# Kernel tuning notes

Hardware: AMD Instinct MI355X
Metric: run time of the kernel (lower is better)

Reference implementation:

```python
import jax, jax.numpy as jnp
import numpy as np

B, C_IN, C_OUT, N, T = 32, 64, 192, 307, 24
DILATIONS = (1, 2)
O3 = C_OUT // 3  # out channels per branch


def setup_inputs() -> dict:
    key = jax.random.key(0)
    ks = iter(jax.random.split(key, 32))
    nrm = lambda shape: 0.05 * jax.random.normal(next(ks), shape, dtype=jnp.float32)
    return {
        "x": jax.random.normal(next(ks), (B, C_IN, N, T), dtype=jnp.float32),
        "adj": jax.random.randint(next(ks), (N, N), 0, 2, dtype=jnp.int32),
        "ln_g": jnp.ones((T,), jnp.float32),
        "ln_b": jnp.zeros((T,), jnp.float32),
        "res_W": nrm((C_OUT, C_IN)), "res_b": nrm((C_OUT,)),
        "ca_W1": nrm((T,)), "ca_W2": nrm((N, T)), "ca_W3": nrm((N,)),
        "cc_W": nrm((O3, C_IN)), "cc_b": nrm((O3,)),
        "ta_W1": nrm((N,)), "ta_W2": nrm((C_IN, N)), "ta_W3": nrm((C_IN,)),
        "tc_W0": nrm((O3, C_IN, 1, 2)), "tc_b0": nrm((O3,)),
        "tc_W1": nrm((O3, O3, 1, 2)), "tc_b1": nrm((O3,)),
        "ga_W1": nrm((T,)), "ga_W2": nrm((C_IN, T)), "ga_W3": nrm((C_IN,)),
        "g_W": nrm((O3, C_IN)),
    }


def layer_norm_lastdim(x, g, b, eps=1e-5):
    mu = jnp.mean(x, axis=-1, keepdims=True)
    var = jnp.var(x, axis=-1, keepdims=True)
    return (x - mu) * jax.lax.rsqrt(var + eps) * g + b


def conv1x1(x, W, b):
    # x: [B,C,N,T], W: [O,C]
    return jnp.einsum("oc,bcnt->bont", W, x) + b[None, :, None, None]


def c_attention(x, W1, W2, W3):
    # channel attention over C; x: [B,C,N,T]
    lhs = jnp.einsum("bcn,nt->bct", jnp.einsum("bcnt,t->bcn", x, W1), W2)  # [B,C,T]
    rhs = jnp.einsum("n,bcnt->bct", W3, x)                                  # [B,C,T]
    att = jax.nn.softmax(jnp.einsum("bct,bdt->bcd", lhs, rhs), axis=-1)     # [B,C,C]
    return jnp.einsum("bcd,bdnt->bcnt", att, x)


def t_attention(x, W1, W2, W3):
    # temporal attention over T; x: [B,C,N,T]
    lhs = jnp.einsum("bct,cn->btn", jnp.einsum("bcnt,n->bct", x, W1), W2)   # [B,T,N]
    rhs = jnp.einsum("c,bcnt->bnt", W3, x)                                   # [B,N,T]
    att = jax.nn.softmax(jnp.einsum("btn,bns->bts", lhs, rhs), axis=-1)      # [B,T,T]
    return jnp.einsum("bts,bcns->bcnt", att, x)


def g_attention(x, adj, W1, W2, W3):
    # graph (spatial) attention over N, masked by adjacency; x: [B,C,N,T]
    lhs = jnp.einsum("bcn,ct->bnt", jnp.einsum("bcnt,t->bcn", x, W1), W2)   # [B,N,T]
    rhs = jnp.einsum("c,bcnt->bnt", W3, x)                                   # [B,N,T]
    scores = jnp.einsum("bnt,bmt->bnm", lhs, rhs)                            # [B,N,N]
    scores = jnp.where(adj[None] > 0, scores, jnp.float32(-1e30))
    att = jax.nn.softmax(scores, axis=-1)
    return jnp.einsum("bnm,bcmt->bcnt", att, x)


def causal_conv(x, W, b, d):
    # Conv2d kernel [1,2], dilation [1,d], pad [0,d] + Chomp(d) == left-pad-only causal conv
    y = jax.lax.conv_general_dilated(
        x, W, window_strides=(1, 1), padding=((0, 0), (d, 0)),
        rhs_dilation=(1, d), dimension_numbers=("NCHW", "OIHW", "NCHW"))
    return y + b[None, :, None, None]


def meam_forward(x, adj, ln_g, ln_b, res_W, res_b, ca_W1, ca_W2, ca_W3, cc_W, cc_b,
                 ta_W1, ta_W2, ta_W3, tc_W0, tc_b0, tc_W1, tc_b1,
                 ga_W1, ga_W2, ga_W3, g_W):
    h = layer_norm_lastdim(x, ln_g, ln_b)
    # CACN branch: channel attention + 1x1 conv
    c_out = conv1x1(c_attention(h, ca_W1, ca_W2, ca_W3), cc_W, cc_b)
    # TACN branch: temporal attention + dilated causal convs
    t_out = t_attention(h, ta_W1, ta_W2, ta_W3)
    t_out = causal_conv(t_out, tc_W0, tc_b0, DILATIONS[0])
    t_out = causal_conv(t_out, tc_W1, tc_b1, DILATIONS[1])
    # GACN branch: graph attention + channel mixing
    g_out = jnp.einsum("oc,bcnt->bont", g_W, g_attention(h, adj, ga_W1, ga_W2, ga_W3))
    out = jnp.concatenate([c_out, t_out, g_out], axis=1)  # [B, C_OUT, N, T]
    return jax.nn.relu(out + conv1x1(x, res_W, res_b))


def reference(x, adj, ln_g, ln_b, res_W, res_b, ca_W1, ca_W2, ca_W3, cc_W, cc_b,
              ta_W1, ta_W2, ta_W3, tc_W0, tc_b0, tc_W1, tc_b1,
              ga_W1, ga_W2, ga_W3, g_W):
    return meam_forward(x, adj, ln_g, ln_b, res_W, res_b, ca_W1, ca_W2, ca_W3, cc_W, cc_b,
                        ta_W1, ta_W2, ta_W3, tc_W0, tc_b0, tc_W1, tc_b1,
                        ga_W1, ga_W2, ga_W3, g_W)
```

## Files before the change

### kernel.cpp

```cpp
#include <hip/hip_runtime.h>
#include <hip/hip_bf16.h>

#define BB 32
#define CC 64
#define NN 307
#define TT 24
#define CO 192
#define NT (NN*TT)
#define GO 1536

using bf16 = __hip_bfloat16;
typedef __attribute__((ext_vector_type(8))) short bf16x8;
typedef __attribute__((ext_vector_type(4))) float f32x4;

#define OFF_ln_g   0
#define OFF_ln_b   24
#define OFF_res_W  48
#define OFF_res_b  12336
#define OFF_ca_W1  12528
#define OFF_ca_W2  12552
#define OFF_ca_W3  19920
#define OFF_cc_W   20227
#define OFF_cc_b   24323
#define OFF_ta_W1  24387
#define OFF_ta_W2  24694
#define OFF_ta_W3  44342
#define OFF_tc_W0  44406
#define OFF_tc_b0  52598
#define OFF_tc_W1  52662
#define OFF_tc_b1  60854
#define OFF_ga_W1  60918
#define OFF_ga_W2  60942
#define OFF_ga_W3  62478
#define OFF_g_W    62542
#define W_TOTAL    66638

__device__ __forceinline__ float xload(const void* p, size_t i, int f) {
  return f ? ((const float*)p)[i] : __bfloat162float(((const bf16*)p)[i]);
}
__device__ __forceinline__ void ostore(void* p, size_t i, float v, int f) {
  if (f) ((float*)p)[i] = v; else ((bf16*)p)[i] = __float2bfloat16(v);
}
__device__ __forceinline__ float oload(const void* p, size_t i, int f) {
  return f ? ((const float*)p)[i] : __bfloat162float(((const bf16*)p)[i]);
}

__global__ void MEAM_44787918963464_kernel() {}

__global__ __launch_bounds__(256) void k_probe(const void* lng_raw, int* flag) {
  if (threadIdx.x == 0 && blockIdx.x == 0) {
    unsigned w = *(const unsigned*)lng_raw;
    *flag = (w == 0x3F800000u) ? 1 : 0;
  }
}

__global__ __launch_bounds__(256) void k_cvt_w(
    const void* p0, const void* p1, const void* p2, const void* p3,
    const void* p4, const void* p5, const void* p6, const void* p7,
    const void* p8, const void* p9, const void* p10, const void* p11,
    const void* p12, const void* p13, const void* p14, const void* p15,
    const void* p16, const void* p17, const void* p18, const void* p19,
    const int* flagp, float* dst) {
  int i = blockIdx.x*256 + threadIdx.x;
  if (i >= W_TOTAL) return;
  const void* ps[20] = {p0,p1,p2,p3,p4,p5,p6,p7,p8,p9,p10,p11,p12,p13,p14,p15,p16,p17,p18,p19};
  const int sz[20] = {24,24,12288,192,24,7368,307,4096,64,307,19648,64,8192,64,8192,64,24,1536,64,4096};
  int f = *flagp;
  int s = 0, base = 0;
  while (i >= base + sz[s]) { base += sz[s]; s++; }
  dst[i] = f ? ((const float*)ps[s])[i-base]
             : __bfloat162float(((const bf16*)ps[s])[i-base]);
}

__global__ __launch_bounds__(256) void k_prep_tc(const float* __restrict__ W,
    bf16* __restrict__ Ag, float* __restrict__ tb_bias) {
  int g = blockIdx.x*256 + threadIdx.x;
  if (g >= CC*CC) return;
  int pI = g >> 6, c = g & 63;
  const float* W0 = W + OFF_tc_W0;
  const float* b0 = W + OFF_tc_b0;
  const float* W1 = W + OFF_tc_W1;
  const float* b1 = W + OFF_tc_b1;
  const float* resW = W + OFF_res_W;
  const float* resb = W + OFF_res_b;
  float m0=0.f,m1=0.f,m2=0.f,m3=0.f, bb0=0.f, bb2=0.f;
  for (int o=0;o<CC;o++){
    float a1v = W1[(pI*CC+o)*2], b1v = W1[(pI*CC+o)*2+1];
    float a0v = W0[(o*CC+c)*2],  b0v = W0[(o*CC+c)*2+1];
    m0 += b1v*b0v; m1 += b1v*a0v; m2 += a1v*b0v; m3 += a1v*a0v;
    bb0 += b1v*b0[o]; bb2 += a1v*b0[o];
  }
  Ag[pI*320 + 0*64 + c] = __float2bfloat16(m0);
  Ag[pI*320 + 1*64 + c] = __float2bfloat16(m1);
  Ag[pI*320 + 2*64 + c] = __float2bfloat16(m2);
  Ag[pI*320 + 3*64 + c] = __float2bfloat16(m3);
  Ag[pI*320 + 4*64 + c] = __float2bfloat16(resW[(64+pI)*CC + c]);
  if (c == 0){
    tb_bias[pI]    = b1[pI] + bb0 + resb[64+pI];
    tb_bias[64+pI] = bb2;
  }
}

__global__ __launch_bounds__(256) void k_prep_A(const float* __restrict__ Mc,
    const float* __restrict__ W, bf16* __restrict__ Apre) {
  int idx = blockIdx.x*256 + threadIdx.x;
  if (idx >= BB*192*128) return;
  int b = idx / 24576;
  int rem = idx - b*24576;
  int p2 = rem >> 7, k = rem & 127;
  const float* resW = W + OFF_res_W;
  const float* gW   = W + OFF_g_W;
  float v;
  if (p2 < 64)       v = (k < 64) ? Mc[b*CC*CC + p2*CC + k] : resW[p2*CC + (k-64)];
  else if (p2 < 128) v = (k < 64) ? gW[(p2-64)*CC + k] : 0.f;
  else               v = (k < 64) ? 0.f : resW[p2*CC + (k-64)];
  Apre[idx] = __float2bfloat16(v);
}

__global__ __launch_bounds__(256) void k_lnct(const void* __restrict__ x, const int* flagp,
    const float* __restrict__ W,
    float* __restrict__ mu_a, float* __restrict__ rs_a,
    float* __restrict__ xw1c, float* __restrict__ xw1g,
    float* __restrict__ lhsc, float* __restrict__ rhsc, float* __restrict__ xw1t) {
  int bc = blockIdx.x;
  int tid = threadIdx.x;
  int f = *flagp;
  const float* lng  = W + OFF_ln_g;
  const float* lnb  = W + OFF_ln_b;
  const float* caW1 = W + OFF_ca_W1;
  const float* gaW1 = W + OFF_ga_W1;
  const float* caW2 = W + OFF_ca_W2;
  const float* caW3 = W + OFF_ca_W3;
  const float* taW1 = W + OFF_ta_W1;
  __shared__ float xs[NN*25];
  __shared__ float mus[NN], rss[NN], w1c[NN];
  __shared__ float red[3*240];
  size_t base = (size_t)bc * NT;
  if (f) {
    const float4* xp = (const float4*)((const float*)x + base);
    for (int e=tid; e<NT/4; e+=256){
      float4 q = xp[e];
      int n = e/6; int t0 = e*4 - n*24;
      float* d = &xs[n*25 + t0];
      d[0]=q.x; d[1]=q.y; d[2]=q.z; d[3]=q.w;
    }
  } else {
    const uint4* xp = (const uint4*)((const unsigned short*)x + base);
    for (int e=tid; e<NT/8; e+=256){
      uint4 q = xp[e]; unsigned u[4]={q.x,q.y,q.z,q.w};
      int n = e/3; int t0 = e*8 - n*24;
      float* d = &xs[n*25 + t0];
      #pragma unroll
      for (int k=0;k<4;k++){
        union{unsigned uu;float fl;} lo,hi;
        lo.uu=u[k]<<16; hi.uu=u[k]&0xffff0000u;
        d[k*2]=lo.fl; d[k*2+1]=hi.fl;
      }
    }
  }
  __syncthreads();
  for (int n=tid; n<NN; n+=256){
    const float* row = &xs[n*25];
    float mu=0.f;
    #pragma unroll
    for (int t=0;t<TT;t++) mu += row[t];
    mu *= (1.f/TT);
    float var=0.f;
    #pragma unroll
    for (int t=0;t<TT;t++){ float d=row[t]-mu; var += d*d; }
    var *= (1.f/TT);
    float rs = rsqrtf(var+1e-5f);
    float s1=0.f, s2=0.f;
    #pragma unroll
    for (int t=0;t<TT;t++){
      float hv=(row[t]-mu)*rs*lng[t]+lnb[t];
      s1+=hv*caW1[t]; s2+=hv*gaW1[t];
    }
    mus[n]=mu; rss[n]=rs; w1c[n]=s1;
    int gi = bc*NN+n;
    mu_a[gi]=mu; rs_a[gi]=rs; xw1c[gi]=s1; xw1g[gi]=s2;
  }
  __syncthreads();
  int t = tid % TT, g = tid / TT;
  if (g < 10){
    float gt=lng[t], bt=lnb[t];
    float l=0.f, rr=0.f, xt=0.f;
    for (int n=g; n<NN; n+=10){
      float hv=(xs[n*25+t]-mus[n])*rss[n]*gt+bt;
      l += w1c[n]*caW2[n*TT+t];
      rr+= caW3[n]*hv;
      xt+= taW1[n]*hv;
    }
    red[g*TT+t]=l; red[240+g*TT+t]=rr; red[480+g*TT+t]=xt;
  }
  __syncthreads();
  if (tid < TT){
    float L=0.f,R=0.f,X=0.f;
    #pragma unroll
    for (int g2=0; g2<10; g2++){
      L+=red[g2*TT+tid]; R+=red[240+g2*TT+tid]; X+=red[480+g2*TT+tid];
    }
    lhsc[bc*TT+tid]=L; rhsc[bc*TT+tid]=R; xw1t[bc*TT+tid]=X;
  }
}

__global__ __launch_bounds__(256) void k_prep_bn(const void* __restrict__ x, const int* flagp,
    const float* __restrict__ mu_a, const float* __restrict__ rs_a,
    const float* __restrict__ W, const float* __restrict__ xw1g,
    float* __restrict__ rhst, float* __restrict__ rhsg, float* __restrict__ lhsg) {
  int i = blockIdx.x*256 + threadIdx.x;
  if (i >= BB*NN*TT) return;
  int f = *flagp;
  const float* lng  = W + OFF_ln_g;
  const float* lnb  = W + OFF_ln_b;
  const float* taW3 = W + OFF_ta_W3;
  const float* gaW3 = W + OFF_ga_W3;
  const float* gaW2 = W + OFF_ga_W2;
  int t = i % TT; int n = (i/TT)%NN; int b = i/(NN*TT);
  float gt = lng[t], bt = lnb[t];
  float a=0.f,c2=0.f,d=0.f;
  for (int c=0;c<CC;c++){
    int row = (b*CC+c)*NN + n;
    float hv = (xload(x, (size_t)row*TT+t, f) - mu_a[row]) * rs_a[row] * gt + bt;
    a  += taW3[c]*hv;
    c2 += gaW3[c]*hv;
    d  += xw1g[row]*gaW2[c*TT+t];
  }
  rhst[i]=a; rhsg[i]=c2; lhsg[i]=d;
}

__global__ __launch_bounds__(256) void k_lhs_t(const float* __restrict__ xw1t,
    const float* __restrict__ W, float* __restrict__ lhst) {
  int i = blockIdx.x*256 + threadIdx.x;
  if (i >= BB*TT*NN) return;
  const float* taW2 = W + OFF_ta_W2;
  int n = i % NN; int t = (i/NN)%TT; int b = i/(TT*NN);
  float acc=0.f;
  for (int c=0;c<CC;c++)
    acc += xw1t[(b*CC+c)*TT+t]*taW2[c*NN+n];
  lhst[i]=acc;
}

__global__ __launch_bounds__(256) void k_att_c(const float* __restrict__ lhsc,
    const float* __restrict__ rhsc, const float* __restrict__ W,
    float* __restrict__ Mc) {
  int b = blockIdx.x; int tid = threadIdx.x;
  const float* ccW = W + OFF_cc_W;
  __shared__ float lc[CC*TT], rc[CC*TT], sc[CC*(CC+1)];
  for (int e=tid;e<CC*TT;e+=256){
    lc[e]=lhsc[b*CC*TT+e];
    rc[e]=rhsc[b*CC*TT+e];
  }
  __syncthreads();
  for (int e=tid;e<CC*CC;e+=256){
    int c=e>>6, d=e&63; float s=0.f;
    for (int t=0;t<TT;t++) s += lc[c*TT+t]*rc[d*TT+t];
    sc[c*(CC+1)+d]=s;
  }
  __syncthreads();
  if (tid<CC){
    float mx=-1e30f;
    for (int d=0;d<CC;d++) mx=fmaxf(mx, sc[tid*(CC+1)+d]);
    float sum=0.f;
    for (int d=0;d<CC;d++){ float e2=__expf(sc[tid*(CC+1)+d]-mx); sc[tid*(CC+1)+d]=e2; sum+=e2; }
    float inv=1.f/sum;
    for (int d=0;d<CC;d++) sc[tid*(CC+1)+d]*=inv;
  }
  __syncthreads();
  for (int e=tid;e<CC*CC;e+=256){
    int o=e>>6, d=e&63; float acc=0.f;
    for (int c=0;c<CC;c++) acc += ccW[o*CC+c]*sc[c*(CC+1)+d];
    Mc[b*CC*CC+e]=acc;
  }
}

__global__ __launch_bounds__(256) void k_att_t(const float* __restrict__ lhst,
    const float* __restrict__ rhst, float* __restrict__ attt) {
  int b=blockIdx.x, tid=threadIdx.x;
  __shared__ float sc[TT*TT];
  for (int e=tid;e<TT*TT;e+=256){
    int t=e/TT, s=e%TT;
    float acc=0.f;
    for (int n=0;n<NN;n++)
      acc += lhst[(b*TT+t)*NN+n]*rhst[(b*NN+n)*TT+s];
    sc[e]=acc;
  }
  __syncthreads();
  if (tid < TT){
    float mx=-1e30f;
    for (int s=0;s<TT;s++) mx=fmaxf(mx,sc[tid*TT+s]);
    float sum=0.f;
    for (int s=0;s<TT;s++){ float e=__expf(sc[tid*TT+s]-mx); sc[tid*TT+s]=e; sum+=e; }
    float inv=1.f/sum;
    for (int s=0;s<TT;s++) attt[b*TT*TT + tid*TT + s]=sc[tid*TT+s]*inv;
  }
}

__global__ __launch_bounds__(256) void k_scores_g(const float* __restrict__ lhsg,
    const float* __restrict__ rhsg, const int* __restrict__ adj,
    float* __restrict__ Sg) {
  int mt = blockIdx.x, nt = blockIdx.y, b = blockIdx.z;
  int n0 = nt*64, m0 = mt*64, tid = threadIdx.x;
  __shared__ unsigned short Lh[64*40], Ll[64*40], Rh[64*40], Rl[64*40];
  for (int e=tid; e<64*24; e+=256){
    int r=e/24, t=e-(e/24)*24;
    int gn=n0+r, gm=m0+r;
    float lv = (gn<NN)? lhsg[((size_t)b*NN+gn)*TT+t] : 0.f;
    float rv = (gm<NN)? rhsg[((size_t)b*NN+gm)*TT+t] : 0.f;
    bf16 lh=__float2bfloat16(lv); float lhf=__bfloat162float(lh);
    bf16 llo=__float2bfloat16(lv-lhf);
    bf16 rh=__float2bfloat16(rv); float rhf=__bfloat162float(rh);
    bf16 rlo=__float2bfloat16(rv-rhf);
    Lh[r*40+t]=*(unsigned short*)&lh; Ll[r*40+t]=*(unsigned short*)&llo;
    Rh[r*40+t]=*(unsigned short*)&rh; Rl[r*40+t]=*(unsigned short*)&rlo;
  }
  for (int e=tid; e<64*8; e+=256){
    int r=e>>3, t=24+(e&7);
    Lh[r*40+t]=0; Ll[r*40+t]=0; Rh[r*40+t]=0; Rl[r*40+t]=0;
  }
  __syncthreads();
  int lane=tid&63, w=tid>>6, q=lane>>4, lr=lane&15;
  bf16x8 ah = *(const bf16x8*)&Lh[(w*16+lr)*40 + q*8];
  bf16x8 al = *(const bf16x8*)&Ll[(w*16+lr)*40 + q*8];
  f32x4 z4={0.f,0.f,0.f,0.f};
  f32x4 acc[4]={z4,z4,z4,z4};
  #pragma unroll
  for (int ct=0;ct<4;ct++){
    bf16x8 bh = *(const bf16x8*)&Rh[(ct*16+lr)*40 + q*8];
    bf16x8 bl = *(const bf16x8*)&Rl[(ct*16+lr)*40 + q*8];
    acc[ct]=__builtin_amdgcn_mfma_f32_16x16x32_bf16(ah,bh,acc[ct],0,0,0);
    acc[ct]=__builtin_amdgcn_mfma_f32_16x16x32_bf16(ah,bl,acc[ct],0,0,0);
    acc[ct]=__builtin_amdgcn_mfma_f32_16x16x32_bf16(al,bh,acc[ct],0,0,0);
  }
  #pragma unroll
  for (int ct=0;ct<4;ct++){
    int m = m0 + ct*16 + lr;
    #pragma unroll
    for (int r=0;r<4;r++){
      int n = n0 + w*16 + q*4 + r;
      if (n<NN && m<NN){
        float s = acc[ct][r];
        if (adj[n*NN+m] <= 0) s = -1e30f;
        Sg[((size_t)b*NN+n)*NN+m] = s;
      }
    }
  }
}

__global__ __launch_bounds__(256) void k_smax_g(const float* __restrict__ Sg,
    bf16* __restrict__ attgh) {
  int b = blockIdx.y;
  int n = blockIdx.x*4 + (threadIdx.x>>6);
  int lane = threadIdx.x & 63;
  if (n >= NN) return;
  const float* row = Sg + ((size_t)b*NN+n)*NN;
  float v[5]; float mx = -1e30f;
  #pragma unroll
  for (int i=0;i<5;i++){
    int m = lane + i*64;
    v[i] = (m<NN)? row[m] : -1e30f;
    mx = fmaxf(mx, v[i]);
  }
  #pragma unroll
  for (int off=32; off; off>>=1) mx = fmaxf(mx, __shfl_xor(mx, off));
  float sum = 0.f;
  #pragma unroll
  for (int i=0;i<5;i++){
    int m = lane + i*64;
    float e = (m<NN)? __expf(v[i]-mx) : 0.f;
    v[i]=e; sum += e;
  }
  #pragma unroll
  for (int off=32; off; off>>=1) sum += __shfl_xor(sum, off);
  float inv = 1.f/sum;
  bf16* orow = attgh + ((size_t)b*NN+n)*NN;
  #pragma unroll
  for (int i=0;i<5;i++){
    int m = lane + i*64;
    if (m<NN) orow[m] = __float2bfloat16(v[i]*inv);
  }
}

__global__ __launch_bounds__(256) void k_hgc_mfma(
    const void* __restrict__ x, const int* flagp,
    const float* __restrict__ mu_a, const float* __restrict__ rs_a,
    const float* __restrict__ W, const bf16* __restrict__ Apre,
    bf16* __restrict__ hg, bf16* __restrict__ resg, void* __restrict__ out) {
  int jt = blockIdx.x, b = blockIdx.y, tid = threadIdx.x;
  int f = *flagp;
  int j0 = jt*64;
  const float* lng = W + OFF_ln_g;
  const float* lnb = W + OFF_ln_b;
  const float* ccb = W + OFF_cc_b;
  const float* resb= W + OFF_res_b;
  __shared__ unsigned short Bs[64*128];

  {
    int c = tid >> 2, jg = tid & 3;
    float xv[16];
    int jbase = j0 + jg*16;
    size_t xoff = (size_t)(b*CC + c)*NT + jbase;
    if (jbase + 15 < NT) {
      if (f) {
        const float4* xp = (const float4*)((const float*)x + xoff);
        #pragma unroll
        for (int v=0; v<4; v++){ float4 q = xp[v]; xv[v*4]=q.x; xv[v*4+1]=q.y; xv[v*4+2]=q.z; xv[v*4+3]=q.w; }
      } else {
        const uint4* xp = (const uint4*)((const unsigned short*)x + xoff);
        #pragma unroll
        for (int v=0; v<2; v++){
          uint4 q = xp[v]; unsigned u[4]={q.x,q.y,q.z,q.w};
          #pragma unroll
          for (int kk2=0;kk2<4;kk2++){
            union{unsigned uu;float fl;} lo,hi;
            lo.uu=u[kk2]<<16; hi.uu=u[kk2]&0xffff0000u;
            xv[v*8+kk2*2]=lo.fl; xv[v*8+kk2*2+1]=hi.fl;
          }
        }
      }
    } else {
      #pragma unroll
      for (int i=0;i<16;i++){ int j=jbase+i; xv[i] = (j<NT)? xload(x, xoff+i, f) : 0.f; }
    }
    const float* mu_r = mu_a + (b*CC+c)*NN;
    const float* rs_r = rs_a + (b*CC+c)*NN;
    #pragma unroll
    for (int i=0;i<16;i++){
      int j = jbase + i;
      int jl = jg*16 + i;
      float hv = 0.f, xf = 0.f;
      if (j < NT){
        int n = j / 24, t = j - n*24;
        xf = xv[i];
        hv = (xf - mu_r[n]) * rs_r[n] * lng[t] + lnb[t];
      }
      int cs = c ^ ((jl&7)<<3);
      bf16 hb = __float2bfloat16(hv), xb = __float2bfloat16(xf);
      Bs[jl*128 + cs]      = *(unsigned short*)&hb;
      Bs[jl*128 + cs + 64] = *(unsigned short*)&xb;
    }
  }

  int lane = tid & 63, w = tid >> 6;
  int q = lane >> 4, lr = lane & 15;
  bf16x8 afo[4], afh[2], afr[2];
  {
    const unsigned short* Ab = (const unsigned short*)Apre + (size_t)b*24576;
    const unsigned short* r0 = Ab + (w*16 + lr)*128;
    #pragma unroll
    for (int kc=0;kc<4;kc++) afo[kc] = *(const bf16x8*)&r0[kc*32 + q*8];
    const unsigned short* r1 = Ab + (64 + w*16 + lr)*128;
    #pragma unroll
    for (int kc=0;kc<2;kc++) afh[kc] = *(const bf16x8*)&r1[kc*32 + q*8];
    const unsigned short* r2 = Ab + (128 + w*16 + lr)*128;
    #pragma unroll
    for (int kc=0;kc<2;kc++) afr[kc] = *(const bf16x8*)&r2[(kc+2)*32 + q*8];
  }
  f32x4 z4 = {0.f,0.f,0.f,0.f};
  f32x4 acco[4] = {z4,z4,z4,z4};
  f32x4 acch[4] = {z4,z4,z4,z4};
  f32x4 accr[4] = {z4,z4,z4,z4};
  __syncthreads();

// ... 461 lines not shown
      bf16x8 bfr = *(const bf16x8*)&Xs[(nl*24+t)*64 + cb];
      acc[ct] = __builtin_amdgcn_mfma_f32_16x16x32_bf16(af[8+kc2], bfr, acc[ct], 0,0,0);
    }
  }

  #pragma unroll
  for (int ct=0;ct<12;ct++){
    int col = ct*16 + lr;
    int nl = col/24, t = col - nl*24;
    int nn = n0 + nl;
    if (nn < NN){
      #pragma unroll
      for (int r=0;r<4;r++){
        int pI = w*16 + q*4 + r;
        size_t idx = ((size_t)b*CO + 64 + pI)*NT + (size_t)nn*TT + t;
        float v = acc[ct][r] + tb_bias[pI] + (t>=2 ? tb_bias[64+pI] : 0.f);
        ostore(out, idx, fmaxf(v, 0.f), f);
      }
    }
  }
}

__global__ __launch_bounds__(256) void k_res_final(const void* __restrict__ x, const int* flagp,
    const float* __restrict__ W, void* __restrict__ out) {
  int jt=blockIdx.x, ot=blockIdx.y, b=blockIdx.z; int tid=threadIdx.x;
  int f = *flagp;
  int j0=jt*64, o0=ot*64;
  const float* resW = W + OFF_res_W;
  const float* resb = W + OFF_res_b;
  __shared__ float Ws[CC*64];
  __shared__ float Xs[CC*64];
  for (int e=tid;e<CC*64;e+=256){
    int o=e&63, c=e>>6;
    Ws[e] = resW[(o0+o)*CC + c];
  }
  for (int e=tid;e<CC*64;e+=256){
    int c=e>>6, j=e&63; int jj=j0+j;
    Xs[e] = (jj<NT) ? xload(x, (size_t)(b*CC+c)*NT + jj, f) : 0.f;
  }
  __syncthreads();
  int ti=tid&15, tj=tid>>4;
  float acc[4][4]={};
  for (int k=0;k<CC;k++){
    float4 a4=*(const float4*)&Ws[k*64+ti*4];
    float4 b4=*(const float4*)&Xs[k*64+tj*4];
    float av[4]={a4.x,a4.y,a4.z,a4.w};
    float bv[4]={b4.x,b4.y,b4.z,b4.w};
    for (int i=0;i<4;i++)
      for (int j=0;j<4;j++) acc[i][j]+=av[i]*bv[j];
  }
  for (int i=0;i<4;i++){
    int o=o0+ti*4+i; float bias=resb[o];
    for (int j=0;j<4;j++){
      int jj=j0+tj*4+j;
      if (jj<NT){
        size_t idx=((size_t)b*CO+o)*NT+jj;
        float v = acc[i][j] + bias + oload(out, idx, f);
        ostore(out, idx, fmaxf(v,0.f), f);
      }
    }
  }
}

extern "C" void kernel_launch(void* const* d_in, const int* in_sizes, int n_in,
                              void* d_out, int out_size, void* d_ws, size_t ws_size,
                              hipStream_t stream) {
  const void* x     = d_in[0];
  const int*  adj   = (const int*)d_in[1];
  void* out = d_out;

  float* p = (float*)d_ws;
  int*   flagp = (int*)p; p += 4;
  float* Wf  = p; p += W_TOTAL;
  float* mu_a = p; p += (size_t)BB*CC*NN;
  float* rs_a = p; p += (size_t)BB*CC*NN;
  float* xw1c = p; p += (size_t)BB*CC*NN;
  float* xw1g = p; p += (size_t)BB*CC*NN;
  float* xw1t = p; p += (size_t)BB*CC*TT;
  float* lhsc = p; p += (size_t)BB*CC*TT;
  float* rhsc = p; p += (size_t)BB*CC*TT;
  float* rhst = p; p += (size_t)BB*NN*TT;
  float* rhsg = p; p += (size_t)BB*NN*TT;
  float* lhsg = p; p += (size_t)BB*NN*TT;
  float* lhst = p; p += (size_t)BB*TT*NN;
  float* attt = p; p += (size_t)BB*TT*TT;
  float* Mc   = p; p += (size_t)BB*CC*CC;
  bf16*  Agm  = (bf16*)p; p += 10240;
  float* tb_bias = p; p += 128;
  bf16*  Apre = (bf16*)p; p += (size_t)BB*192*128/2;
  float* Sg   = p; p += (size_t)BB*NN*NN + 16;
  bf16*  attgh = (bf16*)p; p += (size_t)BB*NN*NN/2 + 16;
  bf16*  resg = (bf16*)p; p += (size_t)BB*CC*NT/2 + 16;
  bf16*  hg   = (bf16*)p;
  size_t need = ((char*)(hg + (size_t)BB*NN*GO)) - (char*)d_ws;
  bool gemm_path = (ws_size >= need);

  k_probe<<<dim3(1), dim3(256), 0, stream>>>(d_in[2], flagp);
  k_cvt_w<<<dim3((W_TOTAL+255)/256), dim3(256), 0, stream>>>(
      d_in[2], d_in[3], d_in[4], d_in[5], d_in[6], d_in[7], d_in[8], d_in[9],
      d_in[10], d_in[11], d_in[12], d_in[13], d_in[14], d_in[15], d_in[16],
      d_in[17], d_in[18], d_in[19], d_in[20], d_in[21], flagp, Wf);
  k_lnct<<<dim3(BB*CC), dim3(256), 0, stream>>>(x, flagp, Wf, mu_a, rs_a, xw1c, xw1g, lhsc, rhsc, xw1t);
  k_prep_bn<<<dim3((BB*NN*TT+255)/256), dim3(256), 0, stream>>>(x, flagp, mu_a, rs_a, Wf, xw1g, rhst, rhsg, lhsg);
  k_lhs_t<<<dim3((BB*TT*NN+255)/256), dim3(256), 0, stream>>>(xw1t, Wf, lhst);
  k_att_c<<<dim3(BB), dim3(256), 0, stream>>>(lhsc, rhsc, Wf, Mc);
  k_att_t<<<dim3(BB), dim3(256), 0, stream>>>(lhst, rhst, attt);
  if (gemm_path) {
    k_prep_tc<<<dim3(16), dim3(256), 0, stream>>>(Wf, Agm, tb_bias);
    k_prep_A<<<dim3((BB*192*128+255)/256), dim3(256), 0, stream>>>(Mc, Wf, Apre);
    int ntile = (NN+63)/64;
    k_scores_g<<<dim3(ntile, ntile, BB), dim3(256), 0, stream>>>(lhsg, rhsg, adj, Sg);
    k_smax_g<<<dim3((NN+3)/4, BB), dim3(256), 0, stream>>>(Sg, attgh);
    k_hgc_mfma<<<dim3((NT+63)/64, BB), dim3(256), 0, stream>>>(x, flagp, mu_a, rs_a, Wf, Apre, hg, resg, out);
    k_tb_mfma<<<dim3((NN+7)/8, BB), dim3(256), 0, stream>>>(x, flagp, mu_a, rs_a, Wf, attt, Agm, tb_bias, out);
    k_gemm_g<<<dim3(GO/64, (NN+63)/64, BB), dim3(256), 0, stream>>>(attgh, hg, resg, flagp, out);
  } else {
    k_cmix<<<dim3((NT+63)/64, BB), dim3(256), 0, stream>>>(Mc, x, flagp, mu_a, rs_a, Wf, out);
    k_graph<<<dim3(NN, BB), dim3(256), 0, stream>>>(lhsg, rhsg, adj, x, flagp, mu_a, rs_a, Wf, out);
    k_tbranch<<<dim3((NN+3)/4, BB), dim3(256), 0, stream>>>(x, flagp, mu_a, rs_a, Wf, attt, out, 0);
    k_res_final<<<dim3((NT+63)/64, 3, BB), dim3(256), 0, stream>>>(x, flagp, Wf, out);
  }
}
```

Before: 659.9 us.

## Fuse small prep/attention kernels and compute graph softmax in-register

Folds the dtype probe into weight conversion, merges the two weight-prep kernels into one launch, and merges channel and temporal attention into one two-row grid. The temporal scores are reassociated so that taW2 is contracted with rhst first, which removes the lhst buffer. The graph score kernel now keeps a full 64-row strip of scores in registers and applies masking and softmax there, so the fp32 Sg round-trip through global memory is gone. In exchange it has fewer blocks per batch for graph attention and uses more registers (80 accumulators per thread).

```diff
diff --git a/kernel.cpp b/kernel.cpp
--- a/kernel.cpp
+++ b/kernel.cpp
@@ -47,74 +47,69 @@
 
 __global__ void MEAM_44787918963464_kernel() {}
 
-__global__ __launch_bounds__(256) void k_probe(const void* lng_raw, int* flag) {
-  if (threadIdx.x == 0 && blockIdx.x == 0) {
-    unsigned w = *(const unsigned*)lng_raw;
-    *flag = (w == 0x3F800000u) ? 1 : 0;
-  }
-}
-
 __global__ __launch_bounds__(256) void k_cvt_w(
     const void* p0, const void* p1, const void* p2, const void* p3,
     const void* p4, const void* p5, const void* p6, const void* p7,
     const void* p8, const void* p9, const void* p10, const void* p11,
     const void* p12, const void* p13, const void* p14, const void* p15,
     const void* p16, const void* p17, const void* p18, const void* p19,
-    const int* flagp, float* dst) {
+    int* flagp, float* dst) {
   int i = blockIdx.x*256 + threadIdx.x;
+  unsigned w0 = *(const unsigned*)p0;
+  int f = (w0 == 0x3F800000u) ? 1 : 0;
+  if (i == 0) *flagp = f;
   if (i >= W_TOTAL) return;
   const void* ps[20] = {p0,p1,p2,p3,p4,p5,p6,p7,p8,p9,p10,p11,p12,p13,p14,p15,p16,p17,p18,p19};
   const int sz[20] = {24,24,12288,192,24,7368,307,4096,64,307,19648,64,8192,64,8192,64,24,1536,64,4096};
-  int f = *flagp;
   int s = 0, base = 0;
   while (i >= base + sz[s]) { base += sz[s]; s++; }
   dst[i] = f ? ((const float*)ps[s])[i-base]
              : __bfloat162float(((const bf16*)ps[s])[i-base]);
 }
 
-__global__ __launch_bounds__(256) void k_prep_tc(const float* __restrict__ W,
-    bf16* __restrict__ Ag, float* __restrict__ tb_bias) {
-  int g = blockIdx.x*256 + threadIdx.x;
-  if (g >= CC*CC) return;
-  int pI = g >> 6, c = g & 63;
-  const float* W0 = W + OFF_tc_W0;
-  const float* b0 = W + OFF_tc_b0;
-  const float* W1 = W + OFF_tc_W1;
-  const float* b1 = W + OFF_tc_b1;
-  const float* resW = W + OFF_res_W;
-  const float* resb = W + OFF_res_b;
-  float m0=0.f,m1=0.f,m2=0.f,m3=0.f, bb0=0.f, bb2=0.f;
-  for (int o=0;o<CC;o++){
-    float a1v = W1[(pI*CC+o)*2], b1v = W1[(pI*CC+o)*2+1];
-    float a0v = W0[(o*CC+c)*2],  b0v = W0[(o*CC+c)*2+1];
-    m0 += b1v*b0v; m1 += b1v*a0v; m2 += a1v*b0v; m3 += a1v*a0v;
-    bb0 += b1v*b0[o]; bb2 += a1v*b0[o];
-  }
-  Ag[pI*320 + 0*64 + c] = __float2bfloat16(m0);
-  Ag[pI*320 + 1*64 + c] = __float2bfloat16(m1);
-  Ag[pI*320 + 2*64 + c] = __float2bfloat16(m2);
-  Ag[pI*320 + 3*64 + c] = __float2bfloat16(m3);
-  Ag[pI*320 + 4*64 + c] = __float2bfloat16(resW[(64+pI)*CC + c]);
-  if (c == 0){
-    tb_bias[pI]    = b1[pI] + bb0 + resb[64+pI];
-    tb_bias[64+pI] = bb2;
-  }
-}
-
-__global__ __launch_bounds__(256) void k_prep_A(const float* __restrict__ Mc,
-    const float* __restrict__ W, bf16* __restrict__ Apre) {
-  int idx = blockIdx.x*256 + threadIdx.x;
-  if (idx >= BB*192*128) return;
-  int b = idx / 24576;
-  int rem = idx - b*24576;
-  int p2 = rem >> 7, k = rem & 127;
-  const float* resW = W + OFF_res_W;
-  const float* gW   = W + OFF_g_W;
-  float v;
-  if (p2 < 64)       v = (k < 64) ? Mc[b*CC*CC + p2*CC + k] : resW[p2*CC + (k-64)];
-  else if (p2 < 128) v = (k < 64) ? gW[(p2-64)*CC + k] : 0.f;
-  else               v = (k < 64) ? 0.f : resW[p2*CC + (k-64)];
-  Apre[idx] = __float2bfloat16(v);
+__global__ __launch_bounds__(256) void k_prep_w(const float* __restrict__ W,
+    const float* __restrict__ Mc, bf16* __restrict__ Ag, float* __restrict__ tb_bias,
+    bf16* __restrict__ Apre) {
+  if (blockIdx.x < 16) {
+    int g = blockIdx.x*256 + threadIdx.x;
+    if (g >= CC*CC) return;
+    int pI = g >> 6, c = g & 63;
+    const float* W0 = W + OFF_tc_W0;
+    const float* b0 = W + OFF_tc_b0;
+    const float* W1 = W + OFF_tc_W1;
+    const float* b1 = W + OFF_tc_b1;
+    const float* resW = W + OFF_res_W;
+    const float* resb = W + OFF_res_b;
+    float m0=0.f,m1=0.f,m2=0.f,m3=0.f, bb0=0.f, bb2=0.f;
+    for (int o=0;o<CC;o++){
+      float a1v = W1[(pI*CC+o)*2], b1v = W1[(pI*CC+o)*2+1];
+      float a0v = W0[(o*CC+c)*2],  b0v = W0[(o*CC+c)*2+1];
+      m0 += b1v*b0v; m1 += b1v*a0v; m2 += a1v*b0v; m3 += a1v*a0v;
+      bb0 += b1v*b0[o]; bb2 += a1v*b0[o];
+    }
+    Ag[pI*320 + 0*64 + c] = __float2bfloat16(m0);
+    Ag[pI*320 + 1*64 + c] = __float2bfloat16(m1);
+    Ag[pI*320 + 2*64 + c] = __float2bfloat16(m2);
+    Ag[pI*320 + 3*64 + c] = __float2bfloat16(m3);
+    Ag[pI*320 + 4*64 + c] = __float2bfloat16(resW[(64+pI)*CC + c]);
+    if (c == 0){
+      tb_bias[pI]    = b1[pI] + bb0 + resb[64+pI];
+      tb_bias[64+pI] = bb2;
+    }
+  } else {
+    int idx = (blockIdx.x-16)*256 + threadIdx.x;
+    if (idx >= BB*192*128) return;
+    int b = idx / 24576;
+    int rem = idx - b*24576;
+    int p2 = rem >> 7, k = rem & 127;
+    const float* resW = W + OFF_res_W;
+    const float* gW   = W + OFF_g_W;
+    float v;
+    if (p2 < 64)       v = (k < 64) ? Mc[b*CC*CC + p2*CC + k] : resW[p2*CC + (k-64)];
+    else if (p2 < 128) v = (k < 64) ? gW[(p2-64)*CC + k] : 0.f;
+    else               v = (k < 64) ? 0.f : resW[p2*CC + (k-64)];
+    Apre[idx] = __float2bfloat16(v);
+  }
 }
 
 __global__ __launch_bounds__(256) void k_lnct(const void* __restrict__ x, const int* flagp,
@@ -229,156 +224,185 @@
   rhst[i]=a; rhsg[i]=c2; lhsg[i]=d;
 }
 
-__global__ __launch_bounds__(256) void k_lhs_t(const float* __restrict__ xw1t,
-    const float* __restrict__ W, float* __restrict__ lhst) {
-  int i = blockIdx.x*256 + threadIdx.x;
-  if (i >= BB*TT*NN) return;
-  const float* taW2 = W + OFF_ta_W2;
-  int n = i % NN; int t = (i/NN)%TT; int b = i/(TT*NN);
-  float acc=0.f;
-  for (int c=0;c<CC;c++)
-    acc += xw1t[(b*CC+c)*TT+t]*taW2[c*NN+n];
-  lhst[i]=acc;
-}
-
-__global__ __launch_bounds__(256) void k_att_c(const float* __restrict__ lhsc,
-    const float* __restrict__ rhsc, const float* __restrict__ W,
-    float* __restrict__ Mc) {
+__global__ __launch_bounds__(256) void k_att_ct(const float* __restrict__ lhsc,
+    const float* __restrict__ rhsc, const float* __restrict__ xw1t,
+    const float* __restrict__ rhst, const float* __restrict__ W,
+    float* __restrict__ Mc, float* __restrict__ attt) {
   int b = blockIdx.x; int tid = threadIdx.x;
-  const float* ccW = W + OFF_cc_W;
-  __shared__ float lc[CC*TT], rc[CC*TT], sc[CC*(CC+1)];
-  for (int e=tid;e<CC*TT;e+=256){
-    lc[e]=lhsc[b*CC*TT+e];
-    rc[e]=rhsc[b*CC*TT+e];
-  }
-  __syncthreads();
-  for (int e=tid;e<CC*CC;e+=256){
-    int c=e>>6, d=e&63; float s=0.f;
-    for (int t=0;t<TT;t++) s += lc[c*TT+t]*rc[d*TT+t];
-    sc[c*(CC+1)+d]=s;
-  }
-  __syncthreads();
-  if (tid<CC){
-    float mx=-1e30f;
-    for (int d=0;d<CC;d++) mx=fmaxf(mx, sc[tid*(CC+1)+d]);
-    float sum=0.f;
-    for (int d=0;d<CC;d++){ float e2=__expf(sc[tid*(CC+1)+d]-mx); sc[tid*(CC+1)+d]=e2; sum+=e2; }
-    float inv=1.f/sum;
-    for (int d=0;d<CC;d++) sc[tid*(CC+1)+d]*=inv;
-  }
-  __syncthreads();
-  for (int e=tid;e<CC*CC;e+=256){
-    int o=e>>6, d=e&63; float acc=0.f;
-    for (int c=0;c<CC;c++) acc += ccW[o*CC+c]*sc[c*(CC+1)+d];
-    Mc[b*CC*CC+e]=acc;
-  }
-}
-
-__global__ __launch_bounds__(256) void k_att_t(const float* __restrict__ lhst,
-    const float* __restrict__ rhst, float* __restrict__ attt) {
-  int b=blockIdx.x, tid=threadIdx.x;
-  __shared__ float sc[TT*TT];
-  for (int e=tid;e<TT*TT;e+=256){
-    int t=e/TT, s=e%TT;
-    float acc=0.f;
-    for (int n=0;n<NN;n++)
-      acc += lhst[(b*TT+t)*NN+n]*rhst[(b*NN+n)*TT+s];
-    sc[e]=acc;
-  }
-  __syncthreads();
-  if (tid < TT){
-    float mx=-1e30f;
-    for (int s=0;s<TT;s++) mx=fmaxf(mx,sc[tid*TT+s]);
-    float sum=0.f;
-    for (int s=0;s<TT;s++){ float e=__expf(sc[tid*TT+s]-mx); sc[tid*TT+s]=e; sum+=e; }
-    float inv=1.f/sum;
-    for (int s=0;s<TT;s++) attt[b*TT*TT + tid*TT + s]=sc[tid*TT+s]*inv;
-  }
-}
-
-__global__ __launch_bounds__(256) void k_scores_g(const float* __restrict__ lhsg,
+  __shared__ float shm[11200];
+  if (blockIdx.y == 0) {
+    const float* ccW = W + OFF_cc_W;
+    float* lc = shm;
+    float* rc = shm + 1536;
+    float* sc = shm + 3072;
+    for (int e=tid;e<CC*TT;e+=256){
+      lc[e]=lhsc[b*CC*TT+e];
+      rc[e]=rhsc[b*CC*TT+e];
+    }
+    __syncthreads();
+    for (int e=tid;e<CC*CC;e+=256){
+      int c=e>>6, d=e&63; float s=0.f;
+      for (int t=0;t<TT;t++) s += lc[c*TT+t]*rc[d*TT+t];
+      sc[c*(CC+1)+d]=s;
+    }
+    __syncthreads();
+    if (tid<CC){
+      float mx=-1e30f;
+      for (int d=0;d<CC;d++) mx=fmaxf(mx, sc[tid*(CC+1)+d]);
+      float sum=0.f;
+      for (int d=0;d<CC;d++){ float e2=__expf(sc[tid*(CC+1)+d]-mx); sc[tid*(CC+1)+d]=e2; sum+=e2; }
+      float inv=1.f/sum;
+      for (int d=0;d<CC;d++) sc[tid*(CC+1)+d]*=inv;
+    }
+    __syncthreads();
+    for (int e=tid;e<CC*CC;e+=256){
+      int o=e>>6, d=e&63; float acc=0.f;
+      for (int c=0;c<CC;c++) acc += ccW[o*CC+c]*sc[c*(CC+1)+d];
+      Mc[b*CC*CC+e]=acc;
+    }
+  } else {
+    const float* taW2 = W + OFF_ta_W2;
+    float* rs2 = shm;
+    float* xw  = shm + 7368;
+    float* P   = shm + 8904;
+    float* sc2 = shm + 10440;
+    for (int e=tid;e<NN*TT;e+=256) rs2[e]=rhst[b*NN*TT+e];
+    for (int e=tid;e<CC*TT;e+=256) xw[e]=xw1t[b*CC*TT+e];
+    __syncthreads();
+    for (int e=tid;e<CC*TT;e+=256){
+      int c=e/TT, s=e-(e/TT)*TT;
+      const float* tw = taW2 + c*NN;
+      float acc=0.f;
+      for (int n=0;n<NN;n++) acc += tw[n]*rs2[n*TT+s];
+      P[c*TT+s]=acc;
+    }
+    __syncthreads();
+    for (int e=tid;e<TT*TT;e+=256){
+      int t=e/TT, s=e-(e/TT)*TT;
+      float acc=0.f;
+      for (int c=0;c<CC;c++) acc += xw[c*TT+t]*P[c*TT+s];
+      sc2[e]=acc;
+    }
+    __syncthreads();
+    if (tid < TT){
+      float mx=-1e30f;
+      for (int s=0;s<TT;s++) mx=fmaxf(mx,sc2[tid*TT+s]);
+      float sum=0.f;
+      for (int s=0;s<TT;s++){ float e=__expf(sc2[tid*TT+s]-mx); sc2[tid*TT+s]=e; sum+=e; }
+      float inv=1.f/sum;
+      for (int s=0;s<TT;s++) attt[b*TT*TT + tid*TT + s]=sc2[tid*TT+s]*inv;
+    }
+  }
+}
+
+__global__ __launch_bounds__(256) void k_attg(const float* __restrict__ lhsg,
     const float* __restrict__ rhsg, const int* __restrict__ adj,
-    float* __restrict__ Sg) {
-  int mt = blockIdx.x, nt = blockIdx.y, b = blockIdx.z;
-  int n0 = nt*64, m0 = mt*64, tid = threadIdx.x;
+    bf16* __restrict__ attgh) {
+  int nt = blockIdx.x, b = blockIdx.y;
+  int n0 = nt*64, tid = threadIdx.x;
   __shared__ unsigned short Lh[64*40], Ll[64*40], Rh[64*40], Rl[64*40];
   for (int e=tid; e<64*24; e+=256){
     int r=e/24, t=e-(e/24)*24;
-    int gn=n0+r, gm=m0+r;
+    int gn=n0+r;
     float lv = (gn<NN)? lhsg[((size_t)b*NN+gn)*TT+t] : 0.f;
-    float rv = (gm<NN)? rhsg[((size_t)b*NN+gm)*TT+t] : 0.f;
     bf16 lh=__float2bfloat16(lv); float lhf=__bfloat162float(lh);
     bf16 llo=__float2bfloat16(lv-lhf);
-    bf16 rh=__float2bfloat16(rv); float rhf=__bfloat162float(rh);
-    bf16 rlo=__float2bfloat16(rv-rhf);
     Lh[r*40+t]=*(unsigned short*)&lh; Ll[r*40+t]=*(unsigned short*)&llo;
-    Rh[r*40+t]=*(unsigned short*)&rh; Rl[r*40+t]=*(unsigned short*)&rlo;
   }
   for (int e=tid; e<64*8; e+=256){
     int r=e>>3, t=24+(e&7);
-    Lh[r*40+t]=0; Ll[r*40+t]=0; Rh[r*40+t]=0; Rl[r*40+t]=0;
-  }
-  __syncthreads();
+    Lh[r*40+t]=0; Ll[r*40+t]=0;
+  }
   int lane=tid&63, w=tid>>6, q=lane>>4, lr=lane&15;
-  bf16x8 ah = *(const bf16x8*)&Lh[(w*16+lr)*40 + q*8];
-  bf16x8 al = *(const bf16x8*)&Ll[(w*16+lr)*40 + q*8];
   f32x4 z4={0.f,0.f,0.f,0.f};
-  f32x4 acc[4]={z4,z4,z4,z4};
-  #pragma unroll
-  for (int ct=0;ct<4;ct++){
-    bf16x8 bh = *(const bf16x8*)&Rh[(ct*16+lr)*40 + q*8];
-    bf16x8 bl = *(const bf16x8*)&Rl[(ct*16+lr)*40 + q*8];
-    acc[ct]=__builtin_amdgcn_mfma_f32_16x16x32_bf16(ah,bh,acc[ct],0,0,0);
-    acc[ct]=__builtin_amdgcn_mfma_f32_16x16x32_bf16(ah,bl,acc[ct],0,0,0);
-    acc[ct]=__builtin_amdgcn_mfma_f32_16x16x32_bf16(al,bh,acc[ct],0,0,0);
-  }
-  #pragma unroll
-  for (int ct=0;ct<4;ct++){
-    int m = m0 + ct*16 + lr;
-    #pragma unroll
-    for (int r=0;r<4;r++){
-      int n = n0 + w*16 + q*4 + r;
-      if (n<NN && m<NN){
-        float s = acc[ct][r];
-        if (adj[n*NN+m] <= 0) s = -1e30f;
-        Sg[((size_t)b*NN+n)*NN+m] = s;
-      }
-    }
-  }
-}
-
-__global__ __launch_bounds__(256) void k_smax_g(const float* __restrict__ Sg,
-    bf16* __restrict__ attgh) {
-  int b = blockIdx.y;
-  int n = blockIdx.x*4 + (threadIdx.x>>6);
-  int lane = threadIdx.x & 63;
-  if (n >= NN) return;
-  const float* row = Sg + ((size_t)b*NN+n)*NN;
-  float v[5]; float mx = -1e30f;
-  #pragma unroll
-  for (int i=0;i<5;i++){
-    int m = lane + i*64;
-    v[i] = (m<NN)? row[m] : -1e30f;
-    mx = fmaxf(mx, v[i]);
-  }
-  #pragma unroll
-  for (int off=32; off; off>>=1) mx = fmaxf(mx, __shfl_xor(mx, off));
-  float sum = 0.f;
-  #pragma unroll
-  for (int i=0;i<5;i++){
-    int m = lane + i*64;
-    float e = (m<NN)? __expf(v[i]-mx) : 0.f;
-    v[i]=e; sum += e;
-  }
-  #pragma unroll
-  for (int off=32; off; off>>=1) sum += __shfl_xor(sum, off);
-  float inv = 1.f/sum;
-  bf16* orow = attgh + ((size_t)b*NN+n)*NN;
-  #pragma unroll
-  for (int i=0;i<5;i++){
-    int m = lane + i*64;
-    if (m<NN) orow[m] = __float2bfloat16(v[i]*inv);
-  }
+  f32x4 acc[5][4];
+  #pragma unroll
+  for (int mt=0;mt<5;mt++)
+    #pragma unroll
+    for (int ct=0;ct<4;ct++) acc[mt][ct]=z4;
+  bf16x8 ah, al;
+  for (int mt=0; mt<5; mt++){
+    __syncthreads();
+    int m0 = mt*64;
+    for (int e=tid; e<64*24; e+=256){
+      int r=e/24, t=e-(e/24)*24;
+      int gm=m0+r;
+      float rv = (gm<NN)? rhsg[((size_t)b*NN+gm)*TT+t] : 0.f;
+      bf16 rh=__float2bfloat16(rv); float rhf=__bfloat162float(rh);
+      bf16 rlo=__float2bfloat16(rv-rhf);
+      Rh[r*40+t]=*(unsigned short*)&rh; Rl[r*40+t]=*(unsigned short*)&rlo;
+    }
+    for (int e=tid; e<64*8; e+=256){
+      int r=e>>3, t=24+(e&7);
+      Rh[r*40+t]=0; Rl[r*40+t]=0;
+    }
+    __syncthreads();
+    if (mt == 0){
+      ah = *(const bf16x8*)&Lh[(w*16+lr)*40 + q*8];
+      al = *(const bf16x8*)&Ll[(w*16+lr)*40 + q*8];
+    }
+    #pragma unroll
+    for (int ct=0;ct<4;ct++){
+      bf16x8 bh = *(const bf16x8*)&Rh[(ct*16+lr)*40 + q*8];
+      bf16x8 bl = *(const bf16x8*)&Rl[(ct*16+lr)*40 + q*8];
+      acc[mt][ct]=__builtin_amdgcn_mfma_f32_16x16x32_bf16(ah,bh,acc[mt][ct],0,0,0);
+      acc[mt][ct]=__builtin_amdgcn_mfma_f32_16x16x32_bf16(ah,bl,acc[mt][ct],0,0,0);
+      acc[mt][ct]=__builtin_amdgcn_mfma_f32_16x16x32_bf16(al,bh,acc[mt][ct],0,0,0);
+    }
+  }
+  int nrow[4];
+  #pragma unroll
+  for (int r=0;r<4;r++) nrow[r] = n0 + w*16 + q*4 + r;
+  float mx[4] = {-1e30f,-1e30f,-1e30f,-1e30f};
+  #pragma unroll
+  for (int mt=0;mt<5;mt++){
+    #pragma unroll
+    for (int ct=0;ct<4;ct++){
+      int m = mt*64 + ct*16 + lr;
+      #pragma unroll
+      for (int r=0;r<4;r++){
+        float s = acc[mt][ct][r];
+        bool ok = (m < NN) && (nrow[r] < NN) && (adj[nrow[r]*NN + m] > 0);
+        s = ok ? s : -1e30f;
+        acc[mt][ct][r] = s;
+        mx[r] = fmaxf(mx[r], s);
+      }
+    }
+  }
+  #pragma unroll
+  for (int off=1; off<16; off<<=1)
+    #pragma unroll
+    for (int r=0;r<4;r++) mx[r] = fmaxf(mx[r], __shfl_xor(mx[r], off));
+  float sum[4] = {0.f,0.f,0.f,0.f};
+  #pragma unroll
+  for (int mt=0;mt<5;mt++)
+    #pragma unroll
+    for (int ct=0;ct<4;ct++)
+      #pragma unroll
+      for (int r=0;r<4;r++){
+        float s = acc[mt][ct][r];
+        float e = (s > -1e29f) ? __expf(s - mx[r]) : 0.f;
+        acc[mt][ct][r] = e;
+        sum[r] += e;
+      }
+  #pragma unroll
+  for (int off=1; off<16; off<<=1)
+    #pragma unroll
+    for (int r=0;r<4;r++) sum[r] += __shfl_xor(sum[r], off);
+  float inv[4];
+  #pragma unroll
+  for (int r=0;r<4;r++) inv[r] = 1.f/sum[r];
+  #pragma unroll
+  for (int mt=0;mt<5;mt++)
+    #pragma unroll
+    for (int ct=0;ct<4;ct++){
+      int m = mt*64 + ct*16 + lr;
+      #pragma unroll
+      for (int r=0;r<4;r++){
+        if (m < NN && nrow[r] < NN)
+          attgh[((size_t)b*NN+nrow[r])*NN + m] = __float2bfloat16(acc[mt][ct][r]*inv[r]);
+      }
+    }
 }
 
 __global__ __launch_bounds__(256) void k_hgc_mfma(
@@ -1006,35 +1030,27 @@
   float* rhst = p; p += (size_t)BB*NN*TT;
   float* rhsg = p; p += (size_t)BB*NN*TT;
   float* lhsg = p; p += (size_t)BB*NN*TT;
-  float* lhst = p; p += (size_t)BB*TT*NN;
   float* attt = p; p += (size_t)BB*TT*TT;
   float* Mc   = p; p += (size_t)BB*CC*CC;
   bf16*  Agm  = (bf16*)p; p += 10240;
   float* tb_bias = p; p += 128;
   bf16*  Apre = (bf16*)p; p += (size_t)BB*192*128/2;
-  float* Sg   = p; p += (size_t)BB*NN*NN + 16;
   bf16*  attgh = (bf16*)p; p += (size_t)BB*NN*NN/2 + 16;
   bf16*  resg = (bf16*)p; p += (size_t)BB*CC*NT/2 + 16;
   bf16*  hg   = (bf16*)p;
   size_t need = ((char*)(hg + (size_t)BB*NN*GO)) - (char*)d_ws;
   bool gemm_path = (ws_size >= need);
 
-  k_probe<<<dim3(1), dim3(256), 0, stream>>>(d_in[2], flagp);
   k_cvt_w<<<dim3((W_TOTAL+255)/256), dim3(256), 0, stream>>>(
       d_in[2], d_in[3], d_in[4], d_in[5], d_in[6], d_in[7], d_in[8], d_in[9],
       d_in[10], d_in[11], d_in[12], d_in[13], d_in[14], d_in[15], d_in[16],
       d_in[17], d_in[18], d_in[19], d_in[20], d_in[21], flagp, Wf);
   k_lnct<<<dim3(BB*CC), dim3(256), 0, stream>>>(x, flagp, Wf, mu_a, rs_a, xw1c, xw1g, lhsc, rhsc, xw1t);
   k_prep_bn<<<dim3((BB*NN*TT+255)/256), dim3(256), 0, stream>>>(x, flagp, mu_a, rs_a, Wf, xw1g, rhst, rhsg, lhsg);
-  k_lhs_t<<<dim3((BB*TT*NN+255)/256), dim3(256), 0, stream>>>(xw1t, Wf, lhst);
-  k_att_c<<<dim3(BB), dim3(256), 0, stream>>>(lhsc, rhsc, Wf, Mc);
-  k_att_t<<<dim3(BB), dim3(256), 0, stream>>>(lhst, rhst, attt);
+  k_att_ct<<<dim3(BB, 2), dim3(256), 0, stream>>>(lhsc, rhsc, xw1t, rhst, Wf, Mc, attt);
   if (gemm_path) {
-    k_prep_tc<<<dim3(16), dim3(256), 0, stream>>>(Wf, Agm, tb_bias);
-    k_prep_A<<<dim3((BB*192*128+255)/256), dim3(256), 0, stream>>>(Mc, Wf, Apre);
-    int ntile = (NN+63)/64;
-    k_scores_g<<<dim3(ntile, ntile, BB), dim3(256), 0, stream>>>(lhsg, rhsg, adj, Sg);
-    k_smax_g<<<dim3((NN+3)/4, BB), dim3(256), 0, stream>>>(Sg, attgh);
+    k_prep_w<<<dim3(16 + (BB*192*128+255)/256), dim3(256), 0, stream>>>(Wf, Mc, Agm, tb_bias, Apre);
+    k_attg<<<dim3((NN+63)/64, BB), dim3(256), 0, stream>>>(lhsg, rhsg, adj, attgh);
     k_hgc_mfma<<<dim3((NT+63)/64, BB), dim3(256), 0, stream>>>(x, flagp, mu_a, rs_a, Wf, Apre, hg, resg, out);
     k_tb_mfma<<<dim3((NN+7)/8, BB), dim3(256), 0, stream>>>(x, flagp, mu_a, rs_a, Wf, attt, Agm, tb_bias, out);
     k_gemm_g<<<dim3(GO/64, (NN+63)/64, BB), dim3(256), 0, stream>>>(attgh, hg, resg, flagp, out);
```

New measurement: 689.4 us. +4.5%, slower.

## Tile prep_bn through shared memory with vectorized loads and fold probe into weight conversion

Applied to the files above, without the earlier changes.

Merges the dtype-probe kernel into the weight-conversion kernel, so every thread derives the flag itself and thread 0 writes it, which removes one launch. Rewrites k_prep_bn so each block covers 8 nodes of one batch and stages the x tile plus the per-row mean, rstd and xw1g values in LDS using float4/uint4 loads. This replaces the strided per-thread global reads over channels. Only 192 of 256 threads compute and LDS use is about 55KB, which limits occupancy.

```diff
diff --git a/kernel.cpp b/kernel.cpp
--- a/kernel.cpp
+++ b/kernel.cpp
@@ -47,25 +47,20 @@
 
 __global__ void MEAM_44787918963464_kernel() {}
 
-__global__ __launch_bounds__(256) void k_probe(const void* lng_raw, int* flag) {
-  if (threadIdx.x == 0 && blockIdx.x == 0) {
-    unsigned w = *(const unsigned*)lng_raw;
-    *flag = (w == 0x3F800000u) ? 1 : 0;
-  }
-}
-
 __global__ __launch_bounds__(256) void k_cvt_w(
     const void* p0, const void* p1, const void* p2, const void* p3,
     const void* p4, const void* p5, const void* p6, const void* p7,
     const void* p8, const void* p9, const void* p10, const void* p11,
     const void* p12, const void* p13, const void* p14, const void* p15,
     const void* p16, const void* p17, const void* p18, const void* p19,
-    const int* flagp, float* dst) {
+    int* flagp, float* dst) {
   int i = blockIdx.x*256 + threadIdx.x;
+  unsigned w0 = *(const unsigned*)p0;
+  int f = (w0 == 0x3F800000u) ? 1 : 0;
+  if (i == 0) *flagp = f;
   if (i >= W_TOTAL) return;
   const void* ps[20] = {p0,p1,p2,p3,p4,p5,p6,p7,p8,p9,p10,p11,p12,p13,p14,p15,p16,p17,p18,p19};
   const int sz[20] = {24,24,12288,192,24,7368,307,4096,64,307,19648,64,8192,64,8192,64,24,1536,64,4096};
-  int f = *flagp;
   int s = 0, base = 0;
   while (i >= base + sz[s]) { base += sz[s]; s++; }
   dst[i] = f ? ((const float*)ps[s])[i-base]
@@ -208,25 +203,70 @@
     const float* __restrict__ mu_a, const float* __restrict__ rs_a,
     const float* __restrict__ W, const float* __restrict__ xw1g,
     float* __restrict__ rhst, float* __restrict__ rhsg, float* __restrict__ lhsg) {
-  int i = blockIdx.x*256 + threadIdx.x;
-  if (i >= BB*NN*TT) return;
+  int nc = blockIdx.x, b = blockIdx.y, tid = threadIdx.x;
+  int n0 = nc*8;
   int f = *flagp;
   const float* lng  = W + OFF_ln_g;
   const float* lnb  = W + OFF_ln_b;
   const float* taW3 = W + OFF_ta_W3;
   const float* gaW3 = W + OFF_ga_W3;
   const float* gaW2 = W + OFF_ga_W2;
-  int t = i % TT; int n = (i/TT)%NN; int b = i/(NN*TT);
-  float gt = lng[t], bt = lnb[t];
-  float a=0.f,c2=0.f,d=0.f;
-  for (int c=0;c<CC;c++){
-    int row = (b*CC+c)*NN + n;
-    float hv = (xload(x, (size_t)row*TT+t, f) - mu_a[row]) * rs_a[row] * gt + bt;
-    a  += taW3[c]*hv;
-    c2 += gaW3[c]*hv;
-    d  += xw1g[row]*gaW2[c*TT+t];
-  }
-  rhst[i]=a; rhsg[i]=c2; lhsg[i]=d;
+  __shared__ float xs[CC*192];
+  __shared__ float mu_s[CC*8], rs_s[CC*8], w1g_s[CC*8];
+  bool full = (n0 + 8 <= NN);
+  if (full) {
+    if (f) {
+      for (int e=tid; e<CC*48; e+=256){
+        int c = e/48, r4 = e - (e/48)*48;
+        float4 q = ((const float4*)((const float*)x + (size_t)(b*CC+c)*NT + n0*TT))[r4];
+        float* d = &xs[c*192 + r4*4];
+        d[0]=q.x; d[1]=q.y; d[2]=q.z; d[3]=q.w;
+      }
+    } else {
+      for (int e=tid; e<CC*24; e+=256){
+        int c = e/24, r8 = e - (e/24)*24;
+        uint4 q = ((const uint4*)((const unsigned short*)x + (size_t)(b*CC+c)*NT + n0*TT))[r8];
+        unsigned u[4]={q.x,q.y,q.z,q.w};
+        float* d = &xs[c*192 + r8*8];
+        #pragma unroll
+        for (int k=0;k<4;k++){
+          union{unsigned uu;float fl;} lo,hi;
+          lo.uu=u[k]<<16; hi.uu=u[k]&0xffff0000u;
+          d[k*2]=lo.fl; d[k*2+1]=hi.fl;
+        }
+      }
+    }
+  } else {
+    for (int e=tid; e<CC*192; e+=256){
+      int c = e/192, r = e - (e/192)*192;
+      int n = n0 + r/24;
+      xs[e] = (n<NN) ? xload(x, (size_t)(b*CC+c)*NT + n0*TT + r, f) : 0.f;
+    }
+  }
+  for (int e=tid; e<CC*8; e+=256){
+    int c = e>>3, i = e&7; int n = n0+i;
+    if (n < NN){
+      int r = (b*CC+c)*NN + n;
+      mu_s[e]=mu_a[r]; rs_s[e]=rs_a[r]; w1g_s[e]=xw1g[r];
+    } else { mu_s[e]=0.f; rs_s[e]=0.f; w1g_s[e]=0.f; }
+  }
+  __syncthreads();
+  if (tid < 192){
+    int i = tid/24, t = tid - (tid/24)*24;
+    int n = n0 + i;
+    if (n < NN){
+      float gt = lng[t], bt = lnb[t];
+      float a=0.f, c2=0.f, d=0.f;
+      for (int c=0;c<CC;c++){
+        float hv = (xs[c*192 + tid] - mu_s[c*8+i]) * rs_s[c*8+i] * gt + bt;
+        a  += taW3[c]*hv;
+        c2 += gaW3[c]*hv;
+        d  += w1g_s[c*8+i]*gaW2[c*TT+t];
+      }
+      int o = (b*NN+n)*TT + t;
+      rhst[o]=a; rhsg[o]=c2; lhsg[o]=d;
+    }
+  }
 }
 
 __global__ __launch_bounds__(256) void k_lhs_t(const float* __restrict__ xw1t,
@@ -1019,13 +1059,12 @@
   size_t need = ((char*)(hg + (size_t)BB*NN*GO)) - (char*)d_ws;
   bool gemm_path = (ws_size >= need);
 
-  k_probe<<<dim3(1), dim3(256), 0, stream>>>(d_in[2], flagp);
   k_cvt_w<<<dim3((W_TOTAL+255)/256), dim3(256), 0, stream>>>(
       d_in[2], d_in[3], d_in[4], d_in[5], d_in[6], d_in[7], d_in[8], d_in[9],
       d_in[10], d_in[11], d_in[12], d_in[13], d_in[14], d_in[15], d_in[16],
       d_in[17], d_in[18], d_in[19], d_in[20], d_in[21], flagp, Wf);
   k_lnct<<<dim3(BB*CC), dim3(256), 0, stream>>>(x, flagp, Wf, mu_a, rs_a, xw1c, xw1g, lhsc, rhsc, xw1t);
-  k_prep_bn<<<dim3((BB*NN*TT+255)/256), dim3(256), 0, stream>>>(x, flagp, mu_a, rs_a, Wf, xw1g, rhst, rhsg, lhsg);
+  k_prep_bn<<<dim3((NN+7)/8, BB), dim3(256), 0, stream>>>(x, flagp, mu_a, rs_a, Wf, xw1g, rhst, rhsg, lhsg);
   k_lhs_t<<<dim3((BB*TT*NN+255)/256), dim3(256), 0, stream>>>(xw1t, Wf, lhst);
   k_att_c<<<dim3(BB), dim3(256), 0, stream>>>(lhsc, rhsc, Wf, Mc);
   k_att_t<<<dim3(BB), dim3(256), 0, stream>>>(lhst, rhst, attt);
```

After: 678.5 us. 1.03x slower.
